# Kernel tuning notes

Hardware: AMD Instinct MI355X
Metric: run time of the kernel (lower is better)

The kernel has to match this reference:

```python
import jax, jax.numpy as jnp
import numpy as np

B, K, H, E = 16384, 5, 512, 512


def setup_inputs() -> dict:
    key = jax.random.key(0)
    ks = jax.random.split(key, 6)
    return {
        "query": jax.random.normal(ks[0], (B, H), dtype=jnp.float32),
        "topics": jax.random.normal(ks[1], (B, K, E), dtype=jnp.float32),
        "coverage_vector": jax.random.uniform(ks[2], (B, K), dtype=jnp.float32),
        "Ua": jax.random.normal(ks[3], (H, E), dtype=jnp.float32) * (1.0 / np.sqrt(E)),
        "Wa": jax.random.normal(ks[4], (H, H), dtype=jnp.float32) * (1.0 / np.sqrt(H)),
        "va_w": jax.random.normal(ks[5], (1, H), dtype=jnp.float32) * (1.0 / np.sqrt(H)),
        "va_b": jnp.zeros((1,), dtype=jnp.float32),
    }


def reference(query, topics, coverage_vector, Ua, Wa, va_w, va_b):
    # proj_key for all topics at once: [B, K, H]
    proj_keys = jnp.einsum("bke,he->bkh", topics, Ua)
    # Faithful to original: query is re-projected by Wa each loop iteration,
    # so step i uses Wa^(i+1) @ query.
    q = query
    scores = []
    for i in range(topics.shape[1]):  # K is small & fixed (topics)
        q = q @ Wa.T  # [B, H]
        s = jnp.tanh(q + proj_keys[:, i, :]) @ va_w.T + va_b  # [B, 1]
        scores.append(s[:, 0] * coverage_vector[:, i])  # [B]
    scores = jnp.stack(scores, axis=1)  # [B, K]
    alphas = jax.nn.softmax(scores, axis=1)  # [B, K]
    mt = jnp.einsum("bk,bke->be", alphas, topics)  # [B, E]
    return (mt, alphas)
```

## Files before the change

kernel.cpp:

```cpp
#include <hip/hip_runtime.h>
#include <hip/hip_bf16.h>
#include <stdint.h>

#define B_SZ 16384
#define K_SZ 5
#define H_SZ 512
#define E_SZ 512

typedef _Float16 f16;
typedef _Float16 f16x8 __attribute__((ext_vector_type(8)));
typedef float    f32x4 __attribute__((ext_vector_type(4)));

__device__ __forceinline__ void gload_lds16(const void* g, void* l) {
  __builtin_amdgcn_global_load_lds(
      (const __attribute__((address_space(1))) unsigned int*)g,
      (__attribute__((address_space(3))) unsigned int*)l, 16, 0, 0);
}

__global__ __launch_bounds__(256) void cvt_kernel(const float* __restrict__ src,
                                                  f16* __restrict__ dst, int n8) {
  int i = blockIdx.x * 256 + threadIdx.x;
  if (i >= n8) return;
  size_t o = (size_t)i * 8;
  float4 a = *(const float4*)(src + o);
  float4 b = *(const float4*)(src + o + 4);
  union { f16 h[8]; uint4 u; } u;
  u.h[0] = (f16)a.x; u.h[1] = (f16)a.y; u.h[2] = (f16)a.z; u.h[3] = (f16)a.w;
  u.h[4] = (f16)b.x; u.h[5] = (f16)b.y; u.h[6] = (f16)b.z; u.h[7] = (f16)b.w;
  *(uint4*)(dst + o) = u.u;
}

__global__ __launch_bounds__(256)
void prep_weights(const float* __restrict__ Wa, const float* __restrict__ Ua,
                  f16* __restrict__ Wbig0, f16* __restrict__ Ua_h,
                  f16* __restrict__ WaT) {
  const int t = threadIdx.x;
  int bb = blockIdx.x;
  if (bb < 128) {
    size_t o = ((size_t)bb * 256 + t) * 8;
    float4 a = *(const float4*)(Wa + o);
    float4 b = *(const float4*)(Wa + o + 4);
    union { f16 h[8]; uint4 u; } u;
    u.h[0] = (f16)a.x; u.h[1] = (f16)a.y; u.h[2] = (f16)a.z; u.h[3] = (f16)a.w;
    u.h[4] = (f16)b.x; u.h[5] = (f16)b.y; u.h[6] = (f16)b.z; u.h[7] = (f16)b.w;
    *(uint4*)(Wbig0 + o) = u.u;
  } else if (bb < 256) {
    size_t o = ((size_t)(bb - 128) * 256 + t) * 8;
    float4 a = *(const float4*)(Ua + o);
    float4 b = *(const float4*)(Ua + o + 4);
    union { f16 h[8]; uint4 u; } u;
    u.h[0] = (f16)a.x; u.h[1] = (f16)a.y; u.h[2] = (f16)a.z; u.h[3] = (f16)a.w;
    u.h[4] = (f16)b.x; u.h[5] = (f16)b.y; u.h[6] = (f16)b.z; u.h[7] = (f16)b.w;
    *(uint4*)(Ua_h + o) = u.u;
  } else {
    __shared__ float tile[32][33];
    int blk = bb - 256;
    int bx = blk & 15, by = blk >> 4;
    int tx = t & 31, ty = t >> 5;
    #pragma unroll
    for (int i = 0; i < 32; i += 8)
      tile[ty + i][tx] = Wa[(size_t)(by * 32 + ty + i) * 512 + bx * 32 + tx];
    __syncthreads();
    #pragma unroll
    for (int i = 0; i < 32; i += 8)
      WaT[(size_t)(bx * 32 + ty + i) * 512 + by * 32 + tx] =
          (f16)tile[tx][ty + i];
  }
}

__global__ __launch_bounds__(256)
void gemm_bt(const f16* __restrict__ A, const f16* __restrict__ W,
             f16* __restrict__ Y, int ldA, int ldY, int nTn) {
  __shared__ f16 As[128 * 32];
  __shared__ f16 Bs[128 * 32];
  const int t = threadIdx.x;
  const int l = t & 63, wid = t >> 6;
  const int wm = wid >> 1, wn = wid & 1;
  int bid = blockIdx.x;
  const int nwg = gridDim.x;
  if ((nwg & 7) == 0) bid = (bid & 7) * (nwg >> 3) + (bid >> 3);
  const int n0 = (bid % nTn) * 128;
  const size_t m0 = (size_t)(bid / nTn) * 128;
  const int lrow = l & 15;
  const int lk = (l >> 4) * 8;

  f32x4 acc[4][4] = {};

  for (int k0 = 0; k0 < 512; k0 += 32) {
    #pragma unroll
    for (int p = 0; p < 2; ++p) {
      int c = p * 256 + t;
      int row = c >> 2, seg = c & 3;
      gload_lds16(W + (size_t)(n0 + row) * 512 + k0 + seg * 8,
                  (char*)Bs + c * 16);
      gload_lds16(A + (m0 + row) * (size_t)ldA + k0 + seg * 8,
                  (char*)As + c * 16);
    }
    __syncthreads();

    f16x8 af[4], bf[4];
    #pragma unroll
    for (int mi = 0; mi < 4; ++mi)
      af[mi] = *(const f16x8*)(As + (wm * 64 + mi * 16 + lrow) * 32 + lk);
    #pragma unroll
    for (int ni = 0; ni < 4; ++ni)
      bf[ni] = *(const f16x8*)(Bs + (wn * 64 + ni * 16 + lrow) * 32 + lk);
    #pragma unroll
    for (int mi = 0; mi < 4; ++mi)
      #pragma unroll
      for (int ni = 0; ni < 4; ++ni)
        acc[mi][ni] = __builtin_amdgcn_mfma_f32_16x16x32_f16(
            af[mi], bf[ni], acc[mi][ni], 0, 0, 0);
    __syncthreads();
  }

  #pragma unroll
  for (int mi = 0; mi < 4; ++mi) {
    #pragma unroll
    for (int j = 0; j < 4; ++j) {
      size_t row = m0 + wm * 64 + mi * 16 + ((l >> 4) << 2) + j;
      #pragma unroll
      for (int ni = 0; ni < 4; ++ni) {
        int col = n0 + wn * 64 + ni * 16 + lrow;
        Y[row * (size_t)ldY + col] = (f16)acc[mi][ni][j];
      }
    }
  }
}

__device__ __forceinline__ float fast_tanh(float x) {
  float e = __expf(-2.f * fabsf(x));
  float r = (1.f - e) / (1.f + e);
  return copysignf(r, x);
}

__global__ __launch_bounds__(256)
void fused_score_gemm(const float* __restrict__ topics,
                      const f16* __restrict__ q0h,
                      const f16* __restrict__ Ua_h,
                      const f16* __restrict__ Wbig,
                      const float* __restrict__ va_w,
                      float* __restrict__ partials) {
  __shared__ f16 As[128 * 32];
  __shared__ f16 Bs[128 * 32];
  const int t = threadIdx.x;
  const int l = t & 63, wid = t >> 6;
  const int wm = wid >> 1, wn = wid & 1;
  int bid = blockIdx.x;
  const int nwg = gridDim.x;
  bid = (bid & 7) * (nwg >> 3) + (bid >> 3);
  const int k = bid >> 9;
  const int rem = bid & 511;
  const int mt = rem >> 2, nt = rem & 3;
  const size_t m0 = (size_t)mt * 128;
  const int n0 = nt * 128;
  const int lrow = l & 15;
  const int lk = (l >> 4) * 8;
  const f16* Pk = Wbig + (size_t)k * 512 * 512;

  f32x4 acc[4][4] = {};

  for (int k0 = 0; k0 < 512; k0 += 32) {
    #pragma unroll
    for (int p = 0; p < 2; ++p) {
      int c = p * 256 + t;
      int row = c >> 2, seg = c & 3;
      gload_lds16(Ua_h + (size_t)(n0 + row) * 512 + k0 + seg * 8,
                  (char*)Bs + c * 16);
    }
    #pragma unroll
    for (int p = 0; p < 4; ++p) {
      int c = p * 256 + t;
      int row = c >> 3, seg = c & 7;
      const float4 v = *(const float4*)(
          topics + ((m0 + row) * K_SZ + k) * E_SZ + k0 + seg * 4);
      union { f16 h[4]; uint2 u; } cv;
      cv.h[0] = (f16)v.x; cv.h[1] = (f16)v.y;
      cv.h[2] = (f16)v.z; cv.h[3] = (f16)v.w;
      *(uint2*)((char*)As + row * 64 + seg * 8) = cv.u;
    }
    __syncthreads();

    f16x8 af[4], bf[4];
    #pragma unroll
    for (int mi = 0; mi < 4; ++mi)
      af[mi] = *(const f16x8*)(As + (wm * 64 + mi * 16 + lrow) * 32 + lk);
    #pragma unroll
    for (int ni = 0; ni < 4; ++ni)
      bf[ni] = *(const f16x8*)(Bs + (wn * 64 + ni * 16 + lrow) * 32 + lk);
    #pragma unroll
    for (int mi = 0; mi < 4; ++mi)
      #pragma unroll
      for (int ni = 0; ni < 4; ++ni)
        acc[mi][ni] = __builtin_amdgcn_mfma_f32_16x16x32_f16(
            af[mi], bf[ni], acc[mi][ni], 0, 0, 0);
    __syncthreads();
  }

  for (int k0 = 0; k0 < 512; k0 += 32) {
    #pragma unroll
    for (int p = 0; p < 2; ++p) {
      int c = p * 256 + t;
      int row = c >> 2, seg = c & 3;
      gload_lds16(Pk + (size_t)(n0 + row) * 512 + k0 + seg * 8,
                  (char*)Bs + c * 16);
      gload_lds16(q0h + (m0 + row) * (size_t)H_SZ + k0 + seg * 8,
                  (char*)As + c * 16);
    }
    __syncthreads();

    f16x8 af[4], bf[4];
    #pragma unroll
    for (int mi = 0; mi < 4; ++mi)
      af[mi] = *(const f16x8*)(As + (wm * 64 + mi * 16 + lrow) * 32 + lk);
    #pragma unroll
    for (int ni = 0; ni < 4; ++ni)
      bf[ni] = *(const f16x8*)(Bs + (wn * 64 + ni * 16 + lrow) * 32 + lk);
    #pragma unroll
    for (int mi = 0; mi < 4; ++mi)
      #pragma unroll
      for (int ni = 0; ni < 4; ++ni)
        acc[mi][ni] = __builtin_amdgcn_mfma_f32_16x16x32_f16(
            af[mi], bf[ni], acc[mi][ni], 0, 0, 0);
    __syncthreads();
  }

  const int colbase = n0 + wn * 64 + lrow;
  float va4[4];
  #pragma unroll
  for (int ni = 0; ni < 4; ++ni) va4[ni] = va_w[colbase + ni * 16];

  #pragma unroll
  for (int mi = 0; mi < 4; ++mi) {
    #pragma unroll
    for (int j = 0; j < 4; ++j) {
      float s = 0.f;
      #pragma unroll
      for (int ni = 0; ni < 4; ++ni)
        s += va4[ni] * fast_tanh(acc[mi][ni][j]);
      #pragma unroll
      for (int m = 1; m < 16; m <<= 1) s += __shfl_xor(s, m);
      if (lrow == 0) {
        int row = (int)m0 + wm * 64 + mi * 16 + ((l >> 4) << 2) + j;
        partials[(size_t)(nt * 2 + wn) * (K_SZ * B_SZ) + k * B_SZ + row] = s;
      }
    }
  }
}

__global__ __launch_bounds__(256)
void finalize2(const float* __restrict__ partials,
               const float* __restrict__ topics, const float* __restrict__ cov,
               const float* __restrict__ va_b, float* __restrict__ out) {
  const int wid = threadIdx.x >> 6, l = threadIdx.x & 63;
  const size_t b = (size_t)blockIdx.x * 4 + wid;
  const float vb = va_b[0];

  float s[K_SZ];
  #pragma unroll
  for (int k = 0; k < K_SZ; ++k) {
    float raw = 0.f;
    #pragma unroll
    for (int sl = 0; sl < 8; ++sl)
      raw += partials[(size_t)sl * (K_SZ * B_SZ) + k * B_SZ + b];
    s[k] = (raw + vb) * cov[b * K_SZ + k];
  }

  float m = s[0];
  #pragma unroll
  for (int k = 1; k < K_SZ; ++k) m = fmaxf(m, s[k]);
  float a[K_SZ], d = 0.f;
  #pragma unroll
  for (int k = 0; k < K_SZ; ++k) { a[k] = __expf(s[k] - m); d += a[k]; }
  float inv = 1.f / d;
  #pragma unroll
  for (int k = 0; k < K_SZ; ++k) a[k] *= inv;

  float acc0[4] = {}, acc1[4] = {};
  #pragma unroll
  for (int k = 0; k < K_SZ; ++k) {
    const float* tp = topics + (b * K_SZ + k) * E_SZ + l * 8;
    float4 t0 = *(const float4*)tp;
    float4 t1 = *(const float4*)(tp + 4);
    acc0[0] += a[k] * t0.x; acc0[1] += a[k] * t0.y;
    acc0[2] += a[k] * t0.z; acc0[3] += a[k] * t0.w;
    acc1[0] += a[k] * t1.x; acc1[1] += a[k] * t1.y;
    acc1[2] += a[k] * t1.z; acc1[3] += a[k] * t1.w;
  }
  float* mo = out + b * E_SZ + l * 8;
  *(float4*)mo       = make_float4(acc0[0], acc0[1], acc0[2], acc0[3]);
  *(float4*)(mo + 4) = make_float4(acc1[0], acc1[1], acc1[2], acc1[3]);
  if (l < K_SZ) {
    float av = (l == 0) ? a[0] : (l == 1) ? a[1] : (l == 2) ? a[2]
               : (l == 3) ? a[3] : a[4];
    out[(size_t)B_SZ * E_SZ + b * K_SZ + l] = av;
  }
}

extern "C" void kernel_launch(void* const* d_in, const int* in_sizes, int n_in,
                              void* d_out, int out_size, void* d_ws, size_t ws_size,
                              hipStream_t stream) {
  const float* query  = (const float*)d_in[0];
  const float* topics = (const float*)d_in[1];
  const float* cov    = (const float*)d_in[2];
  const float* Ua     = (const float*)d_in[3];
  const float* Wa     = (const float*)d_in[4];
  const float* va_w   = (const float*)d_in[5];
  const float* va_b   = (const float*)d_in[6];
  float* out = (float*)d_out;

  char* ws = (char*)d_ws;
  size_t off = 0;
  auto alloc = [&](size_t bytes) -> char* {
    char* p = ws + off;
    off += (bytes + 255) & ~(size_t)255;
    return p;
  };
  f16* q0h   = (f16*)alloc((size_t)B_SZ * H_SZ * 2);
  f16* Ua_h  = (f16*)alloc((size_t)H_SZ * E_SZ * 2);
  f16* WaT   = (f16*)alloc((size_t)H_SZ * H_SZ * 2);
  f16* Wbig  = (f16*)alloc((size_t)K_SZ * H_SZ * H_SZ * 2);
  float* partials = (float*)alloc((size_t)8 * K_SZ * B_SZ * 4);

  prep_weights<<<512, 256, 0, stream>>>(Wa, Ua, Wbig, Ua_h, WaT);
  cvt_kernel<<<B_SZ * H_SZ / 8 / 256, 256, 0, stream>>>(query, q0h,
                                                        B_SZ * H_SZ / 8);
  for (int j = 1; j < K_SZ; ++j)
    gemm_bt<<<16, 256, 0, stream>>>(Wbig + (size_t)(j - 1) * H_SZ * H_SZ, WaT,
                                    Wbig + (size_t)j * H_SZ * H_SZ, H_SZ,
                                    H_SZ, 4);
  fused_score_gemm<<<K_SZ * (B_SZ / 128) * (H_SZ / 128), 256, 0, stream>>>(
      topics, q0h, Ua_h, Wbig, va_w, partials);
  finalize2<<<B_SZ / 4, 256, 0, stream>>>(partials, topics, cov, va_b, out);
}
```

Measured before the change: 464.5 us.

## Fuse prep kernels, merge power chain with grid barrier, double-buffer score GEMM

Folds the query fp16 conversion into the weight-prep kernel and replaces the four dependent small GEMM launches with one persistent 16-block kernel that uses a global atomic barrier between power steps. The main fused score GEMM gains double-buffered LDS: the next tile's global loads are issued before the current tile's MFMAs, overlapping memory and compute. This cuts launch overhead and load-latency stalls, at the cost of twice the LDS per block (possibly lower occupancy). The spin barrier also assumes all 16 blocks are co-resident.

New measurement: 481.0 us. 1.04x slower.

```diff
diff --git a/kernel.cpp b/kernel.cpp
--- a/kernel.cpp
+++ b/kernel.cpp
@@ -17,25 +17,20 @@
       (__attribute__((address_space(3))) unsigned int*)l, 16, 0, 0);
 }
 
-__global__ __launch_bounds__(256) void cvt_kernel(const float* __restrict__ src,
-                                                  f16* __restrict__ dst, int n8) {
-  int i = blockIdx.x * 256 + threadIdx.x;
-  if (i >= n8) return;
-  size_t o = (size_t)i * 8;
-  float4 a = *(const float4*)(src + o);
-  float4 b = *(const float4*)(src + o + 4);
-  union { f16 h[8]; uint4 u; } u;
-  u.h[0] = (f16)a.x; u.h[1] = (f16)a.y; u.h[2] = (f16)a.z; u.h[3] = (f16)a.w;
-  u.h[4] = (f16)b.x; u.h[5] = (f16)b.y; u.h[6] = (f16)b.z; u.h[7] = (f16)b.w;
-  *(uint4*)(dst + o) = u.u;
+__device__ __forceinline__ float fast_tanh(float x) {
+  float e = __expf(-2.f * fabsf(x));
+  float r = (1.f - e) / (1.f + e);
+  return copysignf(r, x);
 }
 
 __global__ __launch_bounds__(256)
-void prep_weights(const float* __restrict__ Wa, const float* __restrict__ Ua,
-                  f16* __restrict__ Wbig0, f16* __restrict__ Ua_h,
-                  f16* __restrict__ WaT) {
+void prep_all(const float* __restrict__ Wa, const float* __restrict__ Ua,
+              const float* __restrict__ query, f16* __restrict__ Wbig0,
+              f16* __restrict__ Ua_h, f16* __restrict__ WaT,
+              f16* __restrict__ q0h, unsigned* __restrict__ bar) {
   const int t = threadIdx.x;
-  int bb = blockIdx.x;
+  const int bb = blockIdx.x;
+  if (bb == 0 && t == 0) *bar = 0u;
   if (bb < 128) {
     size_t o = ((size_t)bb * 256 + t) * 8;
     float4 a = *(const float4*)(Wa + o);
@@ -52,7 +47,7 @@
     u.h[0] = (f16)a.x; u.h[1] = (f16)a.y; u.h[2] = (f16)a.z; u.h[3] = (f16)a.w;
     u.h[4] = (f16)b.x; u.h[5] = (f16)b.y; u.h[6] = (f16)b.z; u.h[7] = (f16)b.w;
     *(uint4*)(Ua_h + o) = u.u;
-  } else {
+  } else if (bb < 512) {
     __shared__ float tile[32][33];
     int blk = bb - 256;
     int bx = blk & 15, by = blk >> 4;
@@ -65,73 +60,81 @@
     for (int i = 0; i < 32; i += 8)
       WaT[(size_t)(bx * 32 + ty + i) * 512 + by * 32 + tx] =
           (f16)tile[tx][ty + i];
-  }
+  } else {
+    size_t o = ((size_t)(bb - 512) * 256 + t) * 8;
+    float4 a = *(const float4*)(query + o);
+    float4 b = *(const float4*)(query + o + 4);
+    union { f16 h[8]; uint4 u; } u;
+    u.h[0] = (f16)a.x; u.h[1] = (f16)a.y; u.h[2] = (f16)a.z; u.h[3] = (f16)a.w;
+    u.h[4] = (f16)b.x; u.h[5] = (f16)b.y; u.h[6] = (f16)b.z; u.h[7] = (f16)b.w;
+    *(uint4*)(q0h + o) = u.u;
+  }
+}
+
+__device__ __forceinline__ void gbar(unsigned* cnt, unsigned target) {
+  __syncthreads();
+  if (threadIdx.x == 0) {
+    __threadfence();
+    __hip_atomic_fetch_add(cnt, 1u, __ATOMIC_ACQ_REL, __HIP_MEMORY_SCOPE_AGENT);
+    while (__hip_atomic_load(cnt, __ATOMIC_ACQUIRE,
+                             __HIP_MEMORY_SCOPE_AGENT) < target)
+      __builtin_amdgcn_s_sleep(2);
+    __threadfence();
+  }
+  __syncthreads();
 }
 
 __global__ __launch_bounds__(256)
-void gemm_bt(const f16* __restrict__ A, const f16* __restrict__ W,
-             f16* __restrict__ Y, int ldA, int ldY, int nTn) {
+void power_chain(const f16* __restrict__ WaT, f16* __restrict__ Wbig,
+                 unsigned* __restrict__ bar) {
   __shared__ f16 As[128 * 32];
   __shared__ f16 Bs[128 * 32];
-  const int t = threadIdx.x;
-  const int l = t & 63, wid = t >> 6;
+  const int t = threadIdx.x, l = t & 63, wid = t >> 6;
   const int wm = wid >> 1, wn = wid & 1;
-  int bid = blockIdx.x;
-  const int nwg = gridDim.x;
-  if ((nwg & 7) == 0) bid = (bid & 7) * (nwg >> 3) + (bid >> 3);
-  const int n0 = (bid % nTn) * 128;
-  const size_t m0 = (size_t)(bid / nTn) * 128;
-  const int lrow = l & 15;
-  const int lk = (l >> 4) * 8;
-
-  f32x4 acc[4][4] = {};
-
-  for (int k0 = 0; k0 < 512; k0 += 32) {
-    #pragma unroll
-    for (int p = 0; p < 2; ++p) {
-      int c = p * 256 + t;
-      int row = c >> 2, seg = c & 3;
-      gload_lds16(W + (size_t)(n0 + row) * 512 + k0 + seg * 8,
-                  (char*)Bs + c * 16);
-      gload_lds16(A + (m0 + row) * (size_t)ldA + k0 + seg * 8,
-                  (char*)As + c * 16);
+  const int mt = blockIdx.x >> 2, nt = blockIdx.x & 3;
+  const int m0 = mt * 128, n0 = nt * 128;
+  const int lrow = l & 15, lk = (l >> 4) * 8;
+
+  for (int j = 1; j < K_SZ; ++j) {
+    const f16* A = Wbig + (size_t)(j - 1) * (512 * 512);
+    f16* Y = Wbig + (size_t)j * (512 * 512);
+    f32x4 acc[4][4] = {};
+    for (int k0 = 0; k0 < 512; k0 += 32) {
+      #pragma unroll
+      for (int p = 0; p < 2; ++p) {
+        int c = p * 256 + t, row = c >> 2, seg = c & 3;
+        gload_lds16(WaT + (size_t)(n0 + row) * 512 + k0 + seg * 8,
+                    (char*)Bs + c * 16);
+        gload_lds16(A + (size_t)(m0 + row) * 512 + k0 + seg * 8,
+                    (char*)As + c * 16);
+      }
+      __syncthreads();
+      f16x8 af[4], bf[4];
+      #pragma unroll
+      for (int mi = 0; mi < 4; ++mi)
+        af[mi] = *(const f16x8*)(As + (wm * 64 + mi * 16 + lrow) * 32 + lk);
+      #pragma unroll
+      for (int ni = 0; ni < 4; ++ni)
+        bf[ni] = *(const f16x8*)(Bs + (wn * 64 + ni * 16 + lrow) * 32 + lk);
+      #pragma unroll
+      for (int mi = 0; mi < 4; ++mi)
+        #pragma unroll
+        for (int ni = 0; ni < 4; ++ni)
+          acc[mi][ni] = __builtin_amdgcn_mfma_f32_16x16x32_f16(
+              af[mi], bf[ni], acc[mi][ni], 0, 0, 0);
+      __syncthreads();
     }
-    __syncthreads();
-
-    f16x8 af[4], bf[4];
     #pragma unroll
     for (int mi = 0; mi < 4; ++mi)
-      af[mi] = *(const f16x8*)(As + (wm * 64 + mi * 16 + lrow) * 32 + lk);
-    #pragma unroll
-    for (int ni = 0; ni < 4; ++ni)
-      bf[ni] = *(const f16x8*)(Bs + (wn * 64 + ni * 16 + lrow) * 32 + lk);
-    #pragma unroll
-    for (int mi = 0; mi < 4; ++mi)
-      #pragma unroll
-      for (int ni = 0; ni < 4; ++ni)
-        acc[mi][ni] = __builtin_amdgcn_mfma_f32_16x16x32_f16(
-            af[mi], bf[ni], acc[mi][ni], 0, 0, 0);
-    __syncthreads();
-  }
-
-  #pragma unroll
-  for (int mi = 0; mi < 4; ++mi) {
-    #pragma unroll
-    for (int j = 0; j < 4; ++j) {
-      size_t row = m0 + wm * 64 + mi * 16 + ((l >> 4) << 2) + j;
-      #pragma unroll
-      for (int ni = 0; ni < 4; ++ni) {
-        int col = n0 + wn * 64 + ni * 16 + lrow;
-        Y[row * (size_t)ldY + col] = (f16)acc[mi][ni][j];
+      #pragma unroll
+      for (int j2 = 0; j2 < 4; ++j2) {
+        size_t row = m0 + wm * 64 + mi * 16 + ((l >> 4) << 2) + j2;
+        #pragma unroll
+        for (int ni = 0; ni < 4; ++ni)
+          Y[row * 512 + n0 + wn * 64 + ni * 16 + lrow] = (f16)acc[mi][ni][j2];
       }
-    }
-  }
-}
-
-__device__ __forceinline__ float fast_tanh(float x) {
-  float e = __expf(-2.f * fabsf(x));
-  float r = (1.f - e) / (1.f + e);
-  return copysignf(r, x);
+    if (j < K_SZ - 1) gbar(bar, 16u * (unsigned)j);
+  }
 }
 
 __global__ __launch_bounds__(256)
@@ -141,87 +144,94 @@
                       const f16* __restrict__ Wbig,
                       const float* __restrict__ va_w,
                       float* __restrict__ partials) {
-  __shared__ f16 As[128 * 32];
-  __shared__ f16 Bs[128 * 32];
+  __shared__ f16 As[2][128 * 32];
+  __shared__ f16 Bs[2][128 * 32];
   const int t = threadIdx.x;
   const int l = t & 63, wid = t >> 6;
   const int wm = wid >> 1, wn = wid & 1;
   int bid = blockIdx.x;
   const int nwg = gridDim.x;
   bid = (bid & 7) * (nwg >> 3) + (bid >> 3);
-  const int k = bid >> 9;
+  const int kq = bid >> 9;
   const int rem = bid & 511;
   const int mt = rem >> 2, nt = rem & 3;
   const size_t m0 = (size_t)mt * 128;
   const int n0 = nt * 128;
   const int lrow = l & 15;
   const int lk = (l >> 4) * 8;
-  const f16* Pk = Wbig + (size_t)k * 512 * 512;
-
+  const f16* Pk = Wbig + (size_t)kq * (512 * 512);
+
+  const float* tA = topics + ((m0 + (t >> 3)) * K_SZ + kq) * (size_t)E_SZ +
+                    (t & 7) * 4;
+  const int ldsA1 = (t >> 3) * 64 + (t & 7) * 8;
+  const f16* tB1 = Ua_h + (size_t)(n0 + (t >> 2)) * 512 + (t & 3) * 8;
+  const f16* tB2 = Pk + (size_t)(n0 + (t >> 2)) * 512 + (t & 3) * 8;
+  const f16* tA2 = q0h + (m0 + (t >> 2)) * (size_t)H_SZ + (t & 3) * 8;
+
+  float4 areg[4];
   f32x4 acc[4][4] = {};
 
-  for (int k0 = 0; k0 < 512; k0 += 32) {
+  auto stage1 = [&](int k0, int buf) {
+    #pragma unroll
+    for (int p = 0; p < 2; ++p)
+      gload_lds16(tB1 + (size_t)p * 64 * 512 + k0,
+                  (char*)Bs[buf] + (p * 256 + t) * 16);
+    #pragma unroll
+    for (int p = 0; p < 4; ++p)
+      areg[p] = *(const float4*)(tA + (size_t)p * 32 * K_SZ * E_SZ + k0);
+  };
+  auto write1 = [&](int buf) {
+    #pragma unroll
+    for (int p = 0; p < 4; ++p) {
+      union { f16 h[4]; uint2 u; } cv;
+      cv.h[0] = (f16)areg[p].x; cv.h[1] = (f16)areg[p].y;
+      cv.h[2] = (f16)areg[p].z; cv.h[3] = (f16)areg[p].w;
+      *(uint2*)((char*)As[buf] + p * 2048 + ldsA1) = cv.u;
+    }
+  };
+  auto stage2 = [&](int k0, int buf) {
     #pragma unroll
     for (int p = 0; p < 2; ++p) {
-      int c = p * 256 + t;
-      int row = c >> 2, seg = c & 3;
-      gload_lds16(Ua_h + (size_t)(n0 + row) * 512 + k0 + seg * 8,
-                  (char*)Bs + c * 16);
+      gload_lds16(tB2 + (size_t)p * 64 * 512 + k0,
+                  (char*)Bs[buf] + (p * 256 + t) * 16);
+      gload_lds16(tA2 + (size_t)p * 64 * H_SZ + k0,
+                  (char*)As[buf] + (p * 256 + t) * 16);
     }
-    #pragma unroll
-    for (int p = 0; p < 4; ++p) {
-      int c = p * 256 + t;
-      int row = c >> 3, seg = c & 7;
-      const float4 v = *(const float4*)(
-          topics + ((m0 + row) * K_SZ + k) * E_SZ + k0 + seg * 4);
-      union { f16 h[4]; uint2 u; } cv;
-      cv.h[0] = (f16)v.x; cv.h[1] = (f16)v.y;
-      cv.h[2] = (f16)v.z; cv.h[3] = (f16)v.w;
-      *(uint2*)((char*)As + row * 64 + seg * 8) = cv.u;
-    }
-    __syncthreads();
-
+  };
+  auto compute = [&](int buf) {
     f16x8 af[4], bf[4];
     #pragma unroll
     for (int mi = 0; mi < 4; ++mi)
-      af[mi] = *(const f16x8*)(As + (wm * 64 + mi * 16 + lrow) * 32 + lk);
+      af[mi] = *(const f16x8*)(As[buf] + (wm * 64 + mi * 16 + lrow) * 32 + lk);
     #pragma unroll
     for (int ni = 0; ni < 4; ++ni)
-      bf[ni] = *(const f16x8*)(Bs + (wn * 64 + ni * 16 + lrow) * 32 + lk);
+      bf[ni] = *(const f16x8*)(Bs[buf] + (wn * 64 + ni * 16 + lrow) * 32 + lk);
     #pragma unroll
     for (int mi = 0; mi < 4; ++mi)
       #pragma unroll
       for (int ni = 0; ni < 4; ++ni)
         acc[mi][ni] = __builtin_amdgcn_mfma_f32_16x16x32_f16(
             af[mi], bf[ni], acc[mi][ni], 0, 0, 0);
+  };
+
+  stage1(0, 0);
+  write1(0);
+  __syncthreads();
+
+  #pragma unroll 2
+  for (int i = 0; i < 16; ++i) {
+    const int cur = i & 1;
+    if (i < 15) stage1((i + 1) * 32, cur ^ 1);
+    else        stage2(0, cur ^ 1);
+    compute(cur);
+    if (i < 15) write1(cur ^ 1);
     __syncthreads();
   }
-
-  for (int k0 = 0; k0 < 512; k0 += 32) {
-    #pragma unroll
-    for (int p = 0; p < 2; ++p) {
-      int c = p * 256 + t;
-      int row = c >> 2, seg = c & 3;
-      gload_lds16(Pk + (size_t)(n0 + row) * 512 + k0 + seg * 8,
-                  (char*)Bs + c * 16);
-      gload_lds16(q0h + (m0 + row) * (size_t)H_SZ + k0 + seg * 8,
-                  (char*)As + c * 16);
-    }
-    __syncthreads();
-
-    f16x8 af[4], bf[4];
-    #pragma unroll
-    for (int mi = 0; mi < 4; ++mi)
-      af[mi] = *(const f16x8*)(As + (wm * 64 + mi * 16 + lrow) * 32 + lk);
-    #pragma unroll
-    for (int ni = 0; ni < 4; ++ni)
-      bf[ni] = *(const f16x8*)(Bs + (wn * 64 + ni * 16 + lrow) * 32 + lk);
-    #pragma unroll
-    for (int mi = 0; mi < 4; ++mi)
-      #pragma unroll
-      for (int ni = 0; ni < 4; ++ni)
-        acc[mi][ni] = __builtin_amdgcn_mfma_f32_16x16x32_f16(
-            af[mi], bf[ni], acc[mi][ni], 0, 0, 0);
+  #pragma unroll 2
+  for (int i = 0; i < 16; ++i) {
+    const int cur = i & 1;
+    if (i < 15) stage2((i + 1) * 32, cur ^ 1);
+    compute(cur);
     __syncthreads();
   }
 
@@ -242,7 +252,7 @@
       for (int m = 1; m < 16; m <<= 1) s += __shfl_xor(s, m);
       if (lrow == 0) {
         int row = (int)m0 + wm * 64 + mi * 16 + ((l >> 4) << 2) + j;
-        partials[(size_t)(nt * 2 + wn) * (K_SZ * B_SZ) + k * B_SZ + row] = s;
+        partials[(size_t)(nt * 2 + wn) * (K_SZ * B_SZ) + kq * B_SZ + row] = s;
       }
     }
   }
@@ -321,14 +331,10 @@
   f16* WaT   = (f16*)alloc((size_t)H_SZ * H_SZ * 2);
   f16* Wbig  = (f16*)alloc((size_t)K_SZ * H_SZ * H_SZ * 2);
   float* partials = (float*)alloc((size_t)8 * K_SZ * B_SZ * 4);
-
-  prep_weights<<<512, 256, 0, stream>>>(Wa, Ua, Wbig, Ua_h, WaT);
-  cvt_kernel<<<B_SZ * H_SZ / 8 / 256, 256, 0, stream>>>(query, q0h,
-                                                        B_SZ * H_SZ / 8);
-  for (int j = 1; j < K_SZ; ++j)
-    gemm_bt<<<16, 256, 0, stream>>>(Wbig + (size_t)(j - 1) * H_SZ * H_SZ, WaT,
-                                    Wbig + (size_t)j * H_SZ * H_SZ, H_SZ,
-                                    H_SZ, 4);
+  unsigned* bar   = (unsigned*)alloc(256);
+
+  prep_all<<<4608, 256, 0, stream>>>(Wa, Ua, query, Wbig, Ua_h, WaT, q0h, bar);
+  power_chain<<<16, 256, 0, stream>>>(WaT, Wbig, bar);
   fused_score_gemm<<<K_SZ * (B_SZ / 128) * (H_SZ / 128), 256, 0, stream>>>(
       topics, q0h, Ua_h, Wbig, va_w, partials);
   finalize2<<<B_SZ / 4, 256, 0, stream>>>(partials, topics, cov, va_b, out);
```
